# Kernel optimization log

Measured on AMD Instinct MI355X. Metric: run time of the kernel, lower is better.

Reference implementation:

```python
import jax, jax.numpy as jnp
import numpy as np

NUM_HEADS = 16
ROPE_THETA = 10000.0


def _rope_angles(seq_len, head_dim, dtype):
    # lucidrains rotary_embedding_torch: freqs = theta^(-2i/d) for i in 0..d/2,
    # angles = pos * freq, then each angle repeated twice along last dim (interleaved pairs).
    inv_freq = 1.0 / (ROPE_THETA ** (jnp.arange(0, head_dim, 2, dtype=jnp.float32) / head_dim))
    angles = jnp.arange(seq_len, dtype=jnp.float32)[:, None] * inv_freq  # [N, D/2]
    return jnp.repeat(angles, 2, axis=-1).astype(dtype)  # [N, D]


def _rotate_half(t):
    # interleaved pairs: (x0, x1) -> (-x1, x0)
    t1 = t[..., ::2]
    t2 = t[..., 1::2]
    return jnp.stack([-t2, t1], axis=-1).reshape(t.shape)


def _apply_rope(t, cos, sin):
    # t: [B, H, N, D]; cos/sin: [N, D]
    return t * cos + _rotate_half(t) * sin


def setup_inputs() -> dict:
    key = jax.random.key(0)
    ks = jax.random.split(key, 5)
    B, N, C = 4, 1024, 1024
    return {
        "x": jax.random.normal(ks[0], (B, N, C), dtype=jnp.float32),
        "w_qkv": jax.random.normal(ks[1], (C, 3 * C), dtype=jnp.float32) * (C ** -0.5),
        "b_qkv": jax.random.normal(ks[2], (3 * C,), dtype=jnp.float32) * 0.02,
        "w_proj": jax.random.normal(ks[3], (C, C), dtype=jnp.float32) * (C ** -0.5),
        "b_proj": jax.random.normal(ks[4], (C,), dtype=jnp.float32) * 0.02,
    }


def reference(x, w_qkv, b_qkv, w_proj, b_proj):
    B, N, C = x.shape
    H = NUM_HEADS
    D = C // H

    qkv = x @ w_qkv + b_qkv  # [B, N, 3C]
    qkv = qkv.reshape(B, N, 3, H, D).transpose(2, 0, 3, 1, 4)  # [3, B, H, N, D]
    q, k, v = qkv[0], qkv[1], qkv[2]

    ang = _rope_angles(N, D, x.dtype)
    cos, sin = jnp.cos(ang), jnp.sin(ang)
    q = _apply_rope(q, cos, sin)
    k = _apply_rope(k, cos, sin)

    scale = D ** -0.5  # SDPA default scale
    scores = jnp.einsum("bhqd,bhkd->bhqk", q, k) * scale
    attn = jax.nn.softmax(scores, axis=-1)
    out = jnp.einsum("bhqk,bhkd->bhqd", attn, v)  # [B, H, N, D]

    out = out.transpose(0, 2, 1, 3).reshape(B, N, C)
    return out @ w_proj + b_proj
```

## Files before the change

### kernel.cpp

```cpp
#include <hip/hip_runtime.h>
#include <math.h>

#define BB 4
#define NN 1024
#define CC 1024
#define HH 16
#define DD 64
#define N3 3072

typedef __attribute__((ext_vector_type(8))) short bf16x8;
typedef __attribute__((ext_vector_type(8))) _Float16 f16x8;
typedef __attribute__((ext_vector_type(4))) _Float16 f16x4;
typedef __attribute__((ext_vector_type(4))) float f32x4;
typedef __attribute__((ext_vector_type(4))) unsigned int u32x4;
typedef __attribute__((ext_vector_type(2))) unsigned int u32x2;

struct ushort4_t { unsigned short x, y, z, w; };

static __device__ __forceinline__ unsigned short f2b(float f) {
    union { float f; unsigned int u; } v; v.f = f;
    unsigned int r = (v.u + 0x7fffu + ((v.u >> 16) & 1u)) >> 16;
    return (unsigned short)r;
}

static __device__ __forceinline__ void ldg_lds16(const void* g, void* l) {
    __builtin_amdgcn_global_load_lds(
        (const __attribute__((address_space(1))) unsigned int*)g,
        (__attribute__((address_space(3))) unsigned int*)l, 16, 0, 0);
}

static __device__ __forceinline__ void barx()  { asm volatile("s_barrier" ::: "memory"); }
static __device__ __forceinline__ void wlg0()  { asm volatile("s_waitcnt lgkmcnt(0)" ::: "memory");
                                                 __builtin_amdgcn_sched_barrier(0); }
static __device__ __forceinline__ void wvm8()  { asm volatile("s_waitcnt vmcnt(8)" ::: "memory"); }
static __device__ __forceinline__ void wvm4()  { asm volatile("s_waitcnt vmcnt(4)" ::: "memory"); }
static __device__ __forceinline__ void wvm0()  { asm volatile("s_waitcnt vmcnt(0)" ::: "memory"); }
static __device__ __forceinline__ void wnone() {}

__global__ __launch_bounds__(256) void prep(const float* __restrict__ x,
                                            const float* __restrict__ wq,
                                            const float* __restrict__ wp,
                                            _Float16* __restrict__ Xh,
                                            _Float16* __restrict__ Wqt,
                                            _Float16* __restrict__ Wpt,
                                            float* __restrict__ ct,
                                            float* __restrict__ st) {
    __shared__ __align__(16) _Float16 T[64][72];
    const int blk = blockIdx.x;
    const int t = threadIdx.x;
    if (blk < 4096) {
        int tid = blk * 256 + t;
        float4 v = ((const float4*)x)[tid];
        f16x4 o = {(_Float16)v.x, (_Float16)v.y, (_Float16)v.z, (_Float16)v.w};
        ((f16x4*)Xh)[tid] = o;
    } else if (blk < 5120) {
        const float* src; _Float16* dst; int ns, k0, n0;
        if (blk < 4864) {
            int idx = blk - 4096;
            k0 = (idx & 15) * 64; n0 = (idx >> 4) * 64;
            src = wq; dst = Wqt; ns = N3;
        } else {
            int idx = blk - 4864;
            k0 = (idx & 15) * 64; n0 = (idx >> 4) * 64;
            src = wp; dst = Wpt; ns = 1024;
        }
        {
            const int r  = t >> 2;
            const int cf = (t & 3) * 16;
            const float* sp = src + (size_t)(k0 + r) * ns + n0 + cf;
            float4 v0 = *(const float4*)(sp);
            float4 v1 = *(const float4*)(sp + 4);
            float4 v2 = *(const float4*)(sp + 8);
            float4 v3 = *(const float4*)(sp + 12);
            f16x8 a, b;
            a[0]=(_Float16)v0.x; a[1]=(_Float16)v0.y; a[2]=(_Float16)v0.z; a[3]=(_Float16)v0.w;
            a[4]=(_Float16)v1.x; a[5]=(_Float16)v1.y; a[6]=(_Float16)v1.z; a[7]=(_Float16)v1.w;
            b[0]=(_Float16)v2.x; b[1]=(_Float16)v2.y; b[2]=(_Float16)v2.z; b[3]=(_Float16)v2.w;
            b[4]=(_Float16)v3.x; b[5]=(_Float16)v3.y; b[6]=(_Float16)v3.z; b[7]=(_Float16)v3.w;
            *(f16x8*)&T[r][cf]     = a;
            *(f16x8*)&T[r][cf + 8] = b;
        }
        __syncthreads();
        {
            const int n  = t >> 2;
            const int kc = t & 3;
            f16x8 o0, o1;
            #pragma unroll
            for (int kk = 0; kk < 8; kk++) o0[kk] = T[kc * 16 + kk][n];
            #pragma unroll
            for (int kk = 0; kk < 8; kk++) o1[kk] = T[kc * 16 + 8 + kk][n];
            _Float16* dp = dst + (size_t)(n0 + n) * 1024 + k0 + kc * 16;
            *(f16x8*)dp       = o0;
            *(f16x8*)(dp + 8) = o1;
        }
    } else {
        int tid = (blk - 5120) * 256 + t;
        int n = tid >> 5, i = tid & 31;
        double ang = (double)n * exp2(-(double)i * (13.287712379549449 / 32.0));
        ct[tid] = (float)cos(ang);
        st[tid] = (float)sin(ang);
    }
}

__global__ __launch_bounds__(512, 2) void qkv_mfma(const _Float16* __restrict__ Ah,
                                                   const _Float16* __restrict__ Bt,
                                                   const float* __restrict__ bias,
                                                   const float* __restrict__ cost,
                                                   const float* __restrict__ sint,
                                                   unsigned short* __restrict__ Q,
                                                   unsigned short* __restrict__ K,
                                                   unsigned short* __restrict__ Vtg) {
    __shared__ __align__(16) _Float16 LA[4][128 * 64];
    __shared__ __align__(16) _Float16 LB[4][128 * 64];

    const int t    = threadIdx.x;
    const int lane = t & 63;
    const int w    = t >> 6;
    const int ln   = lane & 15, qd = lane >> 4;
    const int n0   = blockIdx.x * 256;
    const int m0   = blockIdx.y * 256;
    const int wm   = (w >> 2) * 128;
    const int wn   = (w & 3) * 64;

    const int L0 = t >> 3, hc0 = (t & 7) ^ (L0 & 7);
    const int row0 = 2 * L0 + (hc0 >> 2), co0 = (hc0 & 3) * 16;
    const int pp = 512 + t;
    const int L1 = pp >> 3, hc1 = (pp & 7) ^ (L1 & 7);
    const int row1 = 2 * L1 + (hc1 >> 2), co1 = (hc1 & 3) * 16;

    const char* gA = (const char*)Ah;
    const char* gB = (const char*)Bt;
    const size_t aof0 = (size_t)(m0 + row0) * 2048 + co0;
    const size_t aof1 = (size_t)(m0 + row1) * 2048 + co1;
    const size_t bof0 = (size_t)(n0 + row0) * 2048 + co0;
    const size_t bof1 = (size_t)(n0 + row1) * 2048 + co1;
    const int ld0 = (w * 64) * 8;
    const int ld1 = (512 + w * 64) * 8;

#define STAGE_A(kk, SLOT) { ldg_lds16(gA + aof0 + (size_t)(kk) * 64, &LA[SLOT][ld0]); \
                            ldg_lds16(gA + aof1 + (size_t)(kk) * 64, &LA[SLOT][ld1]); }
#define STAGE_B(kk, SLOT) { ldg_lds16(gB + bof0 + (size_t)(kk) * 64, &LB[SLOT][ld0]); \
                            ldg_lds16(gB + bof1 + (size_t)(kk) * 64, &LB[SLOT][ld1]); }

    STAGE_A(0, 0); STAGE_B(0, 0);
    STAGE_A(1, 1); STAGE_B(1, 1);
    STAGE_A(2, 2); STAGE_B(2, 2);
    wvm8();
    barx();

    f32x4 acc[8][4];
    #pragma unroll
    for (int i = 0; i < 8; i++)
        #pragma unroll
        for (int j = 0; j < 4; j++) acc[i][j] = (f32x4){0.f, 0.f, 0.f, 0.f};

    auto frag = [&](const _Float16* Lb, int r, int c) -> f16x8 {
        int idx = ((r >> 1) << 6) + ((((((r & 1) << 2) | c)) ^ ((r >> 1) & 7)) << 3);
        return *(const f16x8*)&Lb[idx];
    };

#define QK_TILE(kk, SLOT, STG, WAITFN) {                                            \
    const _Float16* Ab = LA[SLOT];                                                  \
    const _Float16* Bb = LB[SLOT];                                                  \
    f16x8 af[4], bf[4];                                                             \
    _Pragma("unroll") for (int i = 0; i < 4; i++) af[i] = frag(Ab, wm + i * 16 + ln, qd); \
    _Pragma("unroll") for (int j = 0; j < 4; j++) bf[j] = frag(Bb, wn + j * 16 + ln, qd); \
    if (STG) STAGE_A((kk) + 3, ((kk) + 3) & 3);                                     \
    barx(); wlg0();                                                                 \
    __builtin_amdgcn_s_setprio(1);                                                  \
    _Pragma("unroll") for (int i = 0; i < 4; i++)                                   \
        _Pragma("unroll") for (int j = 0; j < 4; j++)                               \
            acc[i][j] = __builtin_amdgcn_mfma_f32_16x16x32_f16(af[i], bf[j], acc[i][j], 0, 0, 0); \
    __builtin_amdgcn_s_setprio(0);                                                  \
    barx();                                                                         \
    _Pragma("unroll") for (int i = 0; i < 4; i++) af[i] = frag(Ab, wm + 64 + i * 16 + ln, qd); \
    if (STG) STAGE_B((kk) + 3, ((kk) + 3) & 3);                                     \
    WAITFN();                                                                       \
    barx(); wlg0();                                                                 \
    __builtin_amdgcn_s_setprio(1);                                                  \
    _Pragma("unroll") for (int i = 0; i < 4; i++)                                   \
        _Pragma("unroll") for (int j = 0; j < 4; j++)                               \
            acc[4 + i][j] = __builtin_amdgcn_mfma_f32_16x16x32_f16(af[i], bf[j], acc[4 + i][j], 0, 0, 0); \
    __builtin_amdgcn_s_setprio(0);                                                  \
    barx();                                                                         \
}

    for (int k = 0; k < 28; k += 4) {
        QK_TILE(k + 0, 0, 1, wvm8);
        QK_TILE(k + 1, 1, 1, wvm8);
        QK_TILE(k + 2, 2, 1, wvm8);
        QK_TILE(k + 3, 3, 1, wvm8);
    }
    QK_TILE(28, 0, 1, wvm8);
    QK_TILE(29, 1, 0, wvm4);
    QK_TILE(30, 2, 0, wvm0);
    QK_TILE(31, 3, 0, wnone);

#undef QK_TILE
#undef STAGE_A
#undef STAGE_B

    float* LW = (float*)(&LA[0][0]) + w * (16 * 68);
    const int s = (n0 + wn) >> 10;
    const int h = ((n0 + wn) >> 6) & 15;
    const int erow = lane >> 2;
    const int ec0  = (lane & 3) * 16;

    if (s < 2) {
        unsigned short* dst = (s == 0) ? Q : K;
        const float sc0 = (s == 0) ? 0.125f : 1.0f;
        f32x4 bb0 = *(const f32x4*)&bias[n0 + wn + ec0 + 0];
        f32x4 bb1 = *(const f32x4*)&bias[n0 + wn + ec0 + 4];
        f32x4 bb2 = *(const f32x4*)&bias[n0 + wn + ec0 + 8];
        f32x4 bb3 = *(const f32x4*)&bias[n0 + wn + ec0 + 12];
        #pragma unroll
        for (int i = 0; i < 8; i++) {
            #pragma unroll
            for (int j = 0; j < 4; j++)
                #pragma unroll
                for (int reg = 0; reg < 4; reg++)
                    LW[(qd * 4 + reg) * 68 + j * 16 + ln] = acc[i][j][reg];
            wlg0();
            f32x4 v0 = *(const f32x4*)&LW[erow * 68 + ec0 + 0];
            f32x4 v1 = *(const f32x4*)&LW[erow * 68 + ec0 + 4];
            f32x4 v2 = *(const f32x4*)&LW[erow * 68 + ec0 + 8];
            f32x4 v3 = *(const f32x4*)&LW[erow * 68 + ec0 + 12];
            wlg0();
            int row = m0 + wm + i * 16 + erow;
            int b = row >> 10, n = row & 1023;
            f32x4 cs0 = *(const f32x4*)&cost[n * 32 + (ec0 >> 1)];
            f32x4 cs1 = *(const f32x4*)&cost[n * 32 + (ec0 >> 1) + 4];
            f32x4 sn0 = *(const f32x4*)&sint[n * 32 + (ec0 >> 1)];
            f32x4 sn1 = *(const f32x4*)&sint[n * 32 + (ec0 >> 1) + 4];
            cs0 *= sc0; cs1 *= sc0; sn0 *= sc0; sn1 *= sc0;
            v0 += bb0; v1 += bb1; v2 += bb2; v3 += bb3;
            unsigned int pk0, pk1, pk2, pk3, pk4, pk5, pk6, pk7;
#define RP(PK, ve, vo, cs, sn) { float oe = (ve) * (cs) - (vo) * (sn);              \
                                 float oo = (vo) * (cs) + (ve) * (sn);              \
            asm("v_cvt_pk_bf16_f32 %0, %1, %2" : "=v"(PK) : "v"(oe), "v"(oo)); }
            RP(pk0, v0[0], v0[1], cs0[0], sn0[0]);
            RP(pk1, v0[2], v0[3], cs0[1], sn0[1]);
            RP(pk2, v1[0], v1[1], cs0[2], sn0[2]);
            RP(pk3, v1[2], v1[3], cs0[3], sn0[3]);
            RP(pk4, v2[0], v2[1], cs1[0], sn1[0]);
            RP(pk5, v2[2], v2[3], cs1[1], sn1[1]);
            RP(pk6, v3[0], v3[1], cs1[2], sn1[2]);
            RP(pk7, v3[2], v3[3], cs1[3], sn1[3]);
#undef RP
            unsigned short* op = dst + (((size_t)(b * HH + h)) * NN + n) * DD + ec0;
            u32x4 o0; o0[0] = pk0; o0[1] = pk1; o0[2] = pk2; o0[3] = pk3;
            u32x4 o1; o1[0] = pk4; o1[1] = pk5; o1[2] = pk6; o1[3] = pk7;
            *(u32x4*)op = o0;
            *(u32x4*)(op + 8) = o1;
        }
    } else {
        const float bb = bias[n0 + wn + lane];
        #pragma unroll
        for (int i = 0; i < 8; i++) {
            #pragma unroll
            for (int j = 0; j < 4; j++)
                #pragma unroll
                for (int reg = 0; reg < 4; reg++)
                    LW[(qd * 4 + reg) * 68 + j * 16 + ln] = acc[i][j][reg];
            wlg0();
            float e0  = LW[ 0 * 68 + lane] + bb, e1  = LW[ 1 * 68 + lane] + bb;
            float e2  = LW[ 2 * 68 + lane] + bb, e3  = LW[ 3 * 68 + lane] + bb;
            float e4  = LW[ 4 * 68 + lane] + bb, e5  = LW[ 5 * 68 + lane] + bb;
            float e6  = LW[ 6 * 68 + lane] + bb, e7  = LW[ 7 * 68 + lane] + bb;
            float e8  = LW[ 8 * 68 + lane] + bb, e9  = LW[ 9 * 68 + lane] + bb;
            float e10 = LW[10 * 68 + lane] + bb, e11 = LW[11 * 68 + lane] + bb;
            float e12 = LW[12 * 68 + lane] + bb, e13 = LW[13 * 68 + lane] + bb;
            float e14 = LW[14 * 68 + lane] + bb, e15 = LW[15 * 68 + lane] + bb;
            wlg0();
            unsigned int pk0, pk1, pk2, pk3, pk4, pk5, pk6, pk7;
#define CV(PK, a, b_) asm("v_cvt_pk_bf16_f32 %0, %1, %2" : "=v"(PK) : "v"(a), "v"(b_))
            CV(pk0, e0,  e1);  CV(pk1, e2,  e3);
            CV(pk2, e4,  e5);  CV(pk3, e6,  e7);
            CV(pk4, e8,  e9);  CV(pk5, e10, e11);
            CV(pk6, e12, e13); CV(pk7, e14, e15);
#undef CV
            int row0v = m0 + wm + i * 16;
            int b = row0v >> 10, nn = row0v & 1023;
            unsigned short* vp = Vtg + ((size_t)(b * HH + h) * DD + lane) * NN + nn;
            u32x4 o0; o0[0] = pk0; o0[1] = pk1; o0[2] = pk2; o0[3] = pk3;
            u32x4 o1; o1[0] = pk4; o1[1] = pk5; o1[2] = pk6; o1[3] = pk7;
            *(u32x4*)vp = o0;
            *(u32x4*)(vp + 8) = o1;
        }
    }
}

static __device__ __forceinline__ void gemm_body_pipe_n64(const char* gA, const char* gB,
                                                          int m0, int n0,
                                                          _Float16* As0, _Float16* As1,
                                                          _Float16* Bs0, _Float16* Bs1,
                                                          int tid, int ln, int qd,
                                                          int wm, int wn, f32x4 acc[4][2]) {
    const int lrow   = tid >> 3;
    const int lchunk = tid & 7;
    const int swz    = (lchunk ^ (lrow & 7)) * 8;

    u32x4 pa[4], pb[2];

    #pragma unroll
    for (int c = 0; c < 4; c++)
        pa[c] = *(const u32x4*)(gA + (size_t)(m0 + c * 32 + lrow) * 2048 + lchunk * 16);
    #pragma unroll
    for (int c = 0; c < 2; c++)
        pb[c] = *(const u32x4*)(gB + (size_t)(n0 + c * 32 + lrow) * 2048 + lchunk * 16);
    #pragma unroll
    for (int c = 0; c < 4; c++)
        *(u32x4*)&As0[(c * 32 + lrow) * 64 + swz] = pa[c];
    #pragma unroll
    for (int c = 0; c < 2; c++)
        *(u32x4*)&Bs0[(c * 32 + lrow) * 64 + swz] = pb[c];
    #pragma unroll
    for (int c = 0; c < 4; c++)
        pa[c] = *(const u32x4*)(gA + (size_t)(m0 + c * 32 + lrow) * 2048 + 128 + lchunk * 16);
    #pragma unroll
    for (int c = 0; c < 2; c++)
        pb[c] = *(const u32x4*)(gB + (size_t)(n0 + c * 32 + lrow) * 2048 + 128 + lchunk * 16);
    __syncthreads();

    #pragma unroll
    for (int t = 0; t < 16; t++) {
        const _Float16* Ac = (t & 1) ? As1 : As0;
        const _Float16* Bc = (t & 1) ? Bs1 : Bs0;

        #pragma unroll
        for (int kc = 0; kc < 2; kc++) {
            f16x8 af[4], bf[2];
            #pragma unroll
            for (int i = 0; i < 4; i++)
                af[i] = *(const f16x8*)&Ac[(wm + i * 16 + ln) * 64 +
                                           (((kc * 4 + qd) ^ (ln & 7)) * 8)];
            #pragma unroll
            for (int j = 0; j < 2; j++)
                bf[j] = *(const f16x8*)&Bc[(wn + j * 16 + ln) * 64 +
                                           (((kc * 4 + qd) ^ (ln & 7)) * 8)];
            #pragma unroll
            for (int i = 0; i < 4; i++)
                #pragma unroll
                for (int j = 0; j < 2; j++)
                    acc[i][j] = __builtin_amdgcn_mfma_f32_16x16x32_f16(af[i], bf[j],
                                                                       acc[i][j], 0, 0, 0);
        }

        if (t < 15) {
            _Float16* An = (t & 1) ? As0 : As1;
            _Float16* Bn = (t & 1) ? Bs0 : Bs1;
            #pragma unroll
            for (int c = 0; c < 4; c++)
                *(u32x4*)&An[(c * 32 + lrow) * 64 + swz] = pa[c];
            #pragma unroll
            for (int c = 0; c < 2; c++)
                *(u32x4*)&Bn[(c * 32 + lrow) * 64 + swz] = pb[c];
            if (t < 14) {
                size_t ko = (size_t)(t + 2) * 128;
                #pragma unroll
                for (int c = 0; c < 4; c++)
                    pa[c] = *(const u32x4*)(gA + (size_t)(m0 + c * 32 + lrow) * 2048 + ko + lchunk * 16);
                #pragma unroll
                for (int c = 0; c < 2; c++)
                    pb[c] = *(const u32x4*)(gB + (size_t)(n0 + c * 32 + lrow) * 2048 + ko + lchunk * 16);
            }
        }
        __syncthreads();
    }
}

__global__ __launch_bounds__(256, 3) void attn_flash(const unsigned short* __restrict__ Qb,
                                                     const unsigned short* __restrict__ Kb,
                                                     const unsigned short* __restrict__ Vtg,
                                                     _Float16* __restrict__ AO) {
    __shared__ __align__(16) unsigned short Ks[2][64 * 64];
    __shared__ __align__(16) unsigned short Vt[2][64 * 64];
    __shared__ __align__(16) unsigned short Ps[4][32 * 64];

    const int t    = threadIdx.x;
    const int lane = t & 63;
    const int w    = t >> 6;
    const int ln   = lane & 15;
    const int qd   = lane >> 4;

    const int lin  = blockIdx.x;
    const int slot = lin >> 3;
    const int hb   = (lin & 7) + 8 * (slot & 7);
    const int bq   = slot >> 3;
    const int h    = hb & 15;
    const int b    = hb >> 4;

    const size_t base = (size_t)(b * HH + h) * NN * DD;
    const char* Kc = (const char*)(Kb + base);
    const char* Vc = (const char*)(Vtg + base);
    const int xorc = ((lane & 7) ^ (lane >> 3)) * 16;
    const int r8   = lane >> 3;
    const int wrow = w * 16;

    bf16x8 qf[2][2];
    #pragma unroll
    for (int g = 0; g < 2; g++) {
        const unsigned short* qp = Qb + base +
            (size_t)(bq * 128 + w * 32 + g * 16 + ln) * DD + qd * 8;
        qf[g][0] = *(const bf16x8*)qp;
        qf[g][1] = *(const bf16x8*)(qp + 32);
    }

    f32x4 o[2][5];
    #pragma unroll
    for (int g = 0; g < 2; g++)
        #pragma unroll
        for (int x = 0; x < 5; x++) o[g][x] = (f32x4){0.f, 0.f, 0.f, 0.f};

    bf16x8 onesf;
    #pragma unroll
    for (int x = 0; x < 8; x++) onesf[x] = (short)0x3F80;

#define STAGE_K(tile, buf) {                                                     \
    _Pragma("unroll") for (int c = 0; c < 2; c++) {                              \
        int rr = wrow + c * 8 + r8;                                              \
        ldg_lds16(Kc + (size_t)((tile) * 64 + rr) * 128 + xorc,                  \
                  &Ks[buf][(wrow + c * 8) * 64]);                                \
    } }
// ... 57 lines not shown
        }

        {
            bf16x8 pf[2][2];
            #pragma unroll
            for (int g = 0; g < 2; g++) {
                pf[g][0] = *(const bf16x8*)&PsB[(g * 16 + ln) * 64 + ((qd ^ (ln & 7)) * 8)];
                pf[g][1] = *(const bf16x8*)&PsB[(g * 16 + ln) * 64 + (((4 + qd) ^ (ln & 7)) * 8)];
            }
            __builtin_amdgcn_s_setprio(1);
            #pragma unroll
            for (int j = 0; j < 4; j++) {
                bf16x8 v0f = *(const bf16x8*)&VtB[(ln + 16 * j) * 64 + ((qd ^ (ln & 7)) * 8)];
                bf16x8 v1f = *(const bf16x8*)&VtB[(ln + 16 * j) * 64 + (((4 + qd) ^ (ln & 7)) * 8)];
                #pragma unroll
                for (int g = 0; g < 2; g++) {
                    o[g][j] = __builtin_amdgcn_mfma_f32_16x16x32_bf16(pf[g][0], v0f, o[g][j], 0, 0, 0);
                    o[g][j] = __builtin_amdgcn_mfma_f32_16x16x32_bf16(pf[g][1], v1f, o[g][j], 0, 0, 0);
                }
            }
            #pragma unroll
            for (int g = 0; g < 2; g++) {
                o[g][4] = __builtin_amdgcn_mfma_f32_16x16x32_bf16(pf[g][0], onesf, o[g][4], 0, 0, 0);
                o[g][4] = __builtin_amdgcn_mfma_f32_16x16x32_bf16(pf[g][1], onesf, o[g][4], 0, 0, 0);
            }
            __builtin_amdgcn_s_setprio(0);
        }

        barx();

        if (tt < 14) {
            STAGE_K(tt + 2, tt & 1);
            STAGE_V(tt + 2, tt & 1);
        }
    }

#undef STAGE_K
#undef STAGE_V

    #pragma unroll
    for (int g = 0; g < 2; g++)
        #pragma unroll
        for (int r = 0; r < 4; r++) {
            float inv = __builtin_amdgcn_rcpf(o[g][4][r]);
            int q = bq * 128 + w * 32 + g * 16 + qd * 4 + r;
            _Float16* op = AO + (((size_t)b * NN + q) * HH + h) * DD + ln;
            op[0]  = (_Float16)(o[g][0][r] * inv);
            op[16] = (_Float16)(o[g][1][r] * inv);
            op[32] = (_Float16)(o[g][2][r] * inv);
            op[48] = (_Float16)(o[g][3][r] * inv);
        }
}

__global__ __launch_bounds__(256) void proj_mfma(const _Float16* __restrict__ Ah,
                                                 const _Float16* __restrict__ Bt,
                                                 const float* __restrict__ bias,
                                                 float* __restrict__ out) {
    __shared__ __align__(16) _Float16 As[2][128 * 64];
    __shared__ __align__(16) _Float16 Bs[2][64 * 64];
    const int t = threadIdx.x;
    const int lane = t & 63;
    const int w = t >> 6;
    const int ln = lane & 15, qd = lane >> 4;
    const int n0 = blockIdx.x * 64;
    const int m0 = blockIdx.y * 128;
    const int wm = (w >> 1) * 64, wn = (w & 1) * 32;

    f32x4 acc[4][2];
    #pragma unroll
    for (int i = 0; i < 4; i++)
        #pragma unroll
        for (int j = 0; j < 2; j++) acc[i][j] = (f32x4){0.f, 0.f, 0.f, 0.f};

    gemm_body_pipe_n64((const char*)Ah, (const char*)Bt, m0, n0,
                       As[0], As[1], Bs[0], Bs[1], t, ln, qd, wm, wn, acc);

    #pragma unroll
    for (int i = 0; i < 4; i++) {
        #pragma unroll
        for (int reg = 0; reg < 4; reg++) {
            int row = m0 + wm + i * 16 + qd * 4 + reg;
            #pragma unroll
            for (int j = 0; j < 2; j++) {
                int col = n0 + wn + j * 16 + ln;
                out[(size_t)row * 1024 + col] = acc[i][j][reg] + bias[col];
            }
        }
    }
}

extern "C" void kernel_launch(void* const* d_in, const int* in_sizes, int n_in,
                              void* d_out, int out_size, void* d_ws, size_t ws_size,
                              hipStream_t stream) {
    const float* x      = (const float*)d_in[0];
    const float* w_qkv  = (const float*)d_in[1];
    const float* b_qkv  = (const float*)d_in[2];
    const float* w_proj = (const float*)d_in[3];
    const float* b_proj = (const float*)d_in[4];
    float* out = (float*)d_out;

    char* ws = (char*)d_ws;
    _Float16* Xh   = (_Float16*)(ws);
    _Float16* Wqt  = (_Float16*)(ws + (8u << 20));
    _Float16* Wpt  = (_Float16*)(ws + (14u << 20));
    unsigned short* Q  = (unsigned short*)(ws + (16u << 20));
    unsigned short* K  = (unsigned short*)(ws + (24u << 20));
    unsigned short* Vt = (unsigned short*)(ws + (32u << 20));
    _Float16* AOh  = (_Float16*)(ws + (40u << 20));
    float* cost    = (float*)(ws + (48u << 20));
    float* sint    = (float*)(ws + (48u << 20) + (128u << 10));

    prep<<<5248, 256, 0, stream>>>(x, w_qkv, w_proj, Xh, Wqt, Wpt, cost, sint);
    qkv_mfma<<<dim3(12, 16), 512, 0, stream>>>(Xh, Wqt, b_qkv, cost, sint, Q, K, Vt);
    attn_flash<<<512, 256, 0, stream>>>(Q, K, Vt, AOh);
    proj_mfma<<<dim3(16, 32), 256, 0, stream>>>(AOh, Wpt, b_proj, out);
}
```

Before: 164.7 us.

## Retile QKV GEMM to 128x384 blocks with direct-register epilogue

Changes the QKV projection GEMM tile from 256x256 to 128x384 per block, raising the grid from 192 to 256 blocks so more CUs are busy, and merges the two half-tile MFMA phases into one per k-step. The epilogue no longer stages accumulators through LDS. It applies bias and RoPE per element, using a lane shuffle for the rotation pair, and writes scalar bf16 stores for Q/K and 4-element stores for transposed V. In exchange, the epilogue issues many narrow, poorly coalesced global stores and per-element cos/sin loads, and each block reloads its A tile more often.

```diff
diff --git a/kernel.cpp b/kernel.cpp
--- a/kernel.cpp
+++ b/kernel.cpp
@@ -110,49 +110,51 @@
                                                    unsigned short* __restrict__ Q,
                                                    unsigned short* __restrict__ K,
                                                    unsigned short* __restrict__ Vtg) {
-    __shared__ __align__(16) _Float16 LA[4][128 * 64];
-    __shared__ __align__(16) _Float16 LB[4][128 * 64];
+    __shared__ __align__(16) _Float16 LA[4][128 * 32];
+    __shared__ __align__(16) _Float16 LB[4][384 * 32];
 
     const int t    = threadIdx.x;
     const int lane = t & 63;
     const int w    = t >> 6;
     const int ln   = lane & 15, qd = lane >> 4;
-    const int n0   = blockIdx.x * 256;
-    const int m0   = blockIdx.y * 256;
-    const int wm   = (w >> 2) * 128;
-    const int wn   = (w & 3) * 64;
-
-    const int L0 = t >> 3, hc0 = (t & 7) ^ (L0 & 7);
-    const int row0 = 2 * L0 + (hc0 >> 2), co0 = (hc0 & 3) * 16;
-    const int pp = 512 + t;
-    const int L1 = pp >> 3, hc1 = (pp & 7) ^ (L1 & 7);
-    const int row1 = 2 * L1 + (hc1 >> 2), co1 = (hc1 & 3) * 16;
+    const int n0   = blockIdx.x * 384;
+    const int m0   = blockIdx.y * 128;
+    const int wm   = (w >> 2) * 64;
+    const int wn   = (w & 3) * 96;
+
+    const int La = t >> 3, ha = (t & 7) ^ (La & 7);
+    const int rowA = 2 * La + (ha >> 2), coA = (ha & 3) * 16;
+    const int p1 = 512 + t,  Lb1 = p1 >> 3, hb1 = (p1 & 7) ^ (Lb1 & 7);
+    const int p2 = 1024 + t, Lb2 = p2 >> 3, hb2 = (p2 & 7) ^ (Lb2 & 7);
+    const int rowB0 = 2 * La  + (ha  >> 2), coB0 = (ha  & 3) * 16;
+    const int rowB1 = 2 * Lb1 + (hb1 >> 2), coB1 = (hb1 & 3) * 16;
+    const int rowB2 = 2 * Lb2 + (hb2 >> 2), coB2 = (hb2 & 3) * 16;
 
     const char* gA = (const char*)Ah;
     const char* gB = (const char*)Bt;
-    const size_t aof0 = (size_t)(m0 + row0) * 2048 + co0;
-    const size_t aof1 = (size_t)(m0 + row1) * 2048 + co1;
-    const size_t bof0 = (size_t)(n0 + row0) * 2048 + co0;
-    const size_t bof1 = (size_t)(n0 + row1) * 2048 + co1;
-    const int ld0 = (w * 64) * 8;
-    const int ld1 = (512 + w * 64) * 8;
-
-#define STAGE_A(kk, SLOT) { ldg_lds16(gA + aof0 + (size_t)(kk) * 64, &LA[SLOT][ld0]); \
-                            ldg_lds16(gA + aof1 + (size_t)(kk) * 64, &LA[SLOT][ld1]); }
-#define STAGE_B(kk, SLOT) { ldg_lds16(gB + bof0 + (size_t)(kk) * 64, &LB[SLOT][ld0]); \
-                            ldg_lds16(gB + bof1 + (size_t)(kk) * 64, &LB[SLOT][ld1]); }
-
-    STAGE_A(0, 0); STAGE_B(0, 0);
-    STAGE_A(1, 1); STAGE_B(1, 1);
-    STAGE_A(2, 2); STAGE_B(2, 2);
+    const size_t aof  = (size_t)(m0 + rowA)  * 2048 + coA;
+    const size_t bof0 = (size_t)(n0 + rowB0) * 2048 + coB0;
+    const size_t bof1 = (size_t)(n0 + rowB1) * 2048 + coB1;
+    const size_t bof2 = (size_t)(n0 + rowB2) * 2048 + coB2;
+    const int ldA  = (w * 64) * 8;
+    const int ldB0 = (w * 64) * 8;
+    const int ldB1 = (512 + w * 64) * 8;
+    const int ldB2 = (1024 + w * 64) * 8;
+
+#define STAGE(kk, SLOT) { ldg_lds16(gA + aof  + (size_t)(kk) * 64, &LA[SLOT][ldA]);  \
+                          ldg_lds16(gB + bof0 + (size_t)(kk) * 64, &LB[SLOT][ldB0]); \
+                          ldg_lds16(gB + bof1 + (size_t)(kk) * 64, &LB[SLOT][ldB1]); \
+                          ldg_lds16(gB + bof2 + (size_t)(kk) * 64, &LB[SLOT][ldB2]); }
+
+    STAGE(0, 0); STAGE(1, 1); STAGE(2, 2);
     wvm8();
     barx();
 
-    f32x4 acc[8][4];
-    #pragma unroll
-    for (int i = 0; i < 8; i++)
-        #pragma unroll
-        for (int j = 0; j < 4; j++) acc[i][j] = (f32x4){0.f, 0.f, 0.f, 0.f};
+    f32x4 acc[4][6];
+    #pragma unroll
+    for (int i = 0; i < 4; i++)
+        #pragma unroll
+        for (int j = 0; j < 6; j++) acc[i][j] = (f32x4){0.f, 0.f, 0.f, 0.f};
 
     auto frag = [&](const _Float16* Lb, int r, int c) -> f16x8 {
         int idx = ((r >> 1) << 6) + ((((((r & 1) << 2) | c)) ^ ((r >> 1) & 7)) << 3);
@@ -162,25 +164,16 @@
 #define QK_TILE(kk, SLOT, STG, WAITFN) {                                            \
     const _Float16* Ab = LA[SLOT];                                                  \
     const _Float16* Bb = LB[SLOT];                                                  \
-    f16x8 af[4], bf[4];                                                             \
+    f16x8 af[4], bf[6];                                                             \
     _Pragma("unroll") for (int i = 0; i < 4; i++) af[i] = frag(Ab, wm + i * 16 + ln, qd); \
-    _Pragma("unroll") for (int j = 0; j < 4; j++) bf[j] = frag(Bb, wn + j * 16 + ln, qd); \
-    if (STG) STAGE_A((kk) + 3, ((kk) + 3) & 3);                                     \
+    _Pragma("unroll") for (int j = 0; j < 6; j++) bf[j] = frag(Bb, wn + j * 16 + ln, qd); \
+    if (STG) STAGE((kk) + 3, ((kk) + 3) & 3);                                       \
+    WAITFN();               \
     barx(); wlg0();                                                                 \
     __builtin_amdgcn_s_setprio(1);                                                  \
     _Pragma("unroll") for (int i = 0; i < 4; i++)                                   \
-        _Pragma("unroll") for (int j = 0; j < 4; j++)                               \
+        _Pragma("unroll") for (int j = 0; j < 6; j++)                               \
             acc[i][j] = __builtin_amdgcn_mfma_f32_16x16x32_f16(af[i], bf[j], acc[i][j], 0, 0, 0); \
-    __builtin_amdgcn_s_setprio(0);                                                  \
-    barx();                                                                         \
-    _Pragma("unroll") for (int i = 0; i < 4; i++) af[i] = frag(Ab, wm + 64 + i * 16 + ln, qd); \
-    if (STG) STAGE_B((kk) + 3, ((kk) + 3) & 3);                                     \
-    WAITFN();                                                                       \
-    barx(); wlg0();                                                                 \
-    __builtin_amdgcn_s_setprio(1);                                                  \
-    _Pragma("unroll") for (int i = 0; i < 4; i++)                                   \
-        _Pragma("unroll") for (int j = 0; j < 4; j++)                               \
-            acc[4 + i][j] = __builtin_amdgcn_mfma_f32_16x16x32_f16(af[i], bf[j], acc[4 + i][j], 0, 0, 0); \
     __builtin_amdgcn_s_setprio(0);                                                  \
     barx();                                                                         \
 }
@@ -197,95 +190,47 @@
     QK_TILE(31, 3, 0, wnone);
 
 #undef QK_TILE
-#undef STAGE_A
-#undef STAGE_B
-
-    float* LW = (float*)(&LA[0][0]) + w * (16 * 68);
-    const int s = (n0 + wn) >> 10;
-    const int h = ((n0 + wn) >> 6) & 15;
-    const int erow = lane >> 2;
-    const int ec0  = (lane & 3) * 16;
-
-    if (s < 2) {
-        unsigned short* dst = (s == 0) ? Q : K;
-        const float sc0 = (s == 0) ? 0.125f : 1.0f;
-        f32x4 bb0 = *(const f32x4*)&bias[n0 + wn + ec0 + 0];
-        f32x4 bb1 = *(const f32x4*)&bias[n0 + wn + ec0 + 4];
-        f32x4 bb2 = *(const f32x4*)&bias[n0 + wn + ec0 + 8];
-        f32x4 bb3 = *(const f32x4*)&bias[n0 + wn + ec0 + 12];
-        #pragma unroll
-        for (int i = 0; i < 8; i++) {
-            #pragma unroll
-            for (int j = 0; j < 4; j++)
+#undef STAGE
+
+    #pragma unroll
+    for (int j = 0; j < 6; j++) {
+        const int coln = n0 + wn + j * 16;
+        const int s  = coln >> 10;
+        const int h  = (coln >> 6) & 15;
+        const int d0 = coln & 63;
+        const float bb = bias[coln + ln];
+        if (s < 2) {
+            unsigned short* dst = (s == 0) ? Q : K;
+            const float sc0 = (s == 0) ? 0.125f : 1.0f;
+            const int d = d0 + ln;
+            #pragma unroll
+            for (int i = 0; i < 4; i++) {
                 #pragma unroll
-                for (int reg = 0; reg < 4; reg++)
-                    LW[(qd * 4 + reg) * 68 + j * 16 + ln] = acc[i][j][reg];
-            wlg0();
-            f32x4 v0 = *(const f32x4*)&LW[erow * 68 + ec0 + 0];
-            f32x4 v1 = *(const f32x4*)&LW[erow * 68 + ec0 + 4];
-            f32x4 v2 = *(const f32x4*)&LW[erow * 68 + ec0 + 8];
-            f32x4 v3 = *(const f32x4*)&LW[erow * 68 + ec0 + 12];
-            wlg0();
-            int row = m0 + wm + i * 16 + erow;
-            int b = row >> 10, n = row & 1023;
-            f32x4 cs0 = *(const f32x4*)&cost[n * 32 + (ec0 >> 1)];
-            f32x4 cs1 = *(const f32x4*)&cost[n * 32 + (ec0 >> 1) + 4];
-            f32x4 sn0 = *(const f32x4*)&sint[n * 32 + (ec0 >> 1)];
-            f32x4 sn1 = *(const f32x4*)&sint[n * 32 + (ec0 >> 1) + 4];
-            cs0 *= sc0; cs1 *= sc0; sn0 *= sc0; sn1 *= sc0;
-            v0 += bb0; v1 += bb1; v2 += bb2; v3 += bb3;
-            unsigned int pk0, pk1, pk2, pk3, pk4, pk5, pk6, pk7;
-#define RP(PK, ve, vo, cs, sn) { float oe = (ve) * (cs) - (vo) * (sn);              \
-                                 float oo = (vo) * (cs) + (ve) * (sn);              \
-            asm("v_cvt_pk_bf16_f32 %0, %1, %2" : "=v"(PK) : "v"(oe), "v"(oo)); }
-            RP(pk0, v0[0], v0[1], cs0[0], sn0[0]);
-            RP(pk1, v0[2], v0[3], cs0[1], sn0[1]);
-            RP(pk2, v1[0], v1[1], cs0[2], sn0[2]);
-            RP(pk3, v1[2], v1[3], cs0[3], sn0[3]);
-            RP(pk4, v2[0], v2[1], cs1[0], sn1[0]);
-            RP(pk5, v2[2], v2[3], cs1[1], sn1[1]);
-            RP(pk6, v3[0], v3[1], cs1[2], sn1[2]);
-            RP(pk7, v3[2], v3[3], cs1[3], sn1[3]);
-#undef RP
-            unsigned short* op = dst + (((size_t)(b * HH + h)) * NN + n) * DD + ec0;
-            u32x4 o0; o0[0] = pk0; o0[1] = pk1; o0[2] = pk2; o0[3] = pk3;
-            u32x4 o1; o1[0] = pk4; o1[1] = pk5; o1[2] = pk6; o1[3] = pk7;
-            *(u32x4*)op = o0;
-            *(u32x4*)(op + 8) = o1;
-        }
-    } else {
-        const float bb = bias[n0 + wn + lane];
-        #pragma unroll
-        for (int i = 0; i < 8; i++) {
-            #pragma unroll
-            for (int j = 0; j < 4; j++)
-                #pragma unroll
-                for (int reg = 0; reg < 4; reg++)
-                    LW[(qd * 4 + reg) * 68 + j * 16 + ln] = acc[i][j][reg];
-            wlg0();
-            float e0  = LW[ 0 * 68 + lane] + bb, e1  = LW[ 1 * 68 + lane] + bb;
-            float e2  = LW[ 2 * 68 + lane] + bb, e3  = LW[ 3 * 68 + lane] + bb;
-            float e4  = LW[ 4 * 68 + lane] + bb, e5  = LW[ 5 * 68 + lane] + bb;
-            float e6  = LW[ 6 * 68 + lane] + bb, e7  = LW[ 7 * 68 + lane] + bb;
-            float e8  = LW[ 8 * 68 + lane] + bb, e9  = LW[ 9 * 68 + lane] + bb;
-            float e10 = LW[10 * 68 + lane] + bb, e11 = LW[11 * 68 + lane] + bb;
-            float e12 = LW[12 * 68 + lane] + bb, e13 = LW[13 * 68 + lane] + bb;
-            float e14 = LW[14 * 68 + lane] + bb, e15 = LW[15 * 68 + lane] + bb;
-            wlg0();
-            unsigned int pk0, pk1, pk2, pk3, pk4, pk5, pk6, pk7;
-#define CV(PK, a, b_) asm("v_cvt_pk_bf16_f32 %0, %1, %2" : "=v"(PK) : "v"(a), "v"(b_))
-            CV(pk0, e0,  e1);  CV(pk1, e2,  e3);
-            CV(pk2, e4,  e5);  CV(pk3, e6,  e7);
-            CV(pk4, e8,  e9);  CV(pk5, e10, e11);
-            CV(pk6, e12, e13); CV(pk7, e14, e15);
-#undef CV
-            int row0v = m0 + wm + i * 16;
-            int b = row0v >> 10, nn = row0v & 1023;
-            unsigned short* vp = Vtg + ((size_t)(b * HH + h) * DD + lane) * NN + nn;
-            u32x4 o0; o0[0] = pk0; o0[1] = pk1; o0[2] = pk2; o0[3] = pk3;
-            u32x4 o1; o1[0] = pk4; o1[1] = pk5; o1[2] = pk6; o1[3] = pk7;
-            *(u32x4*)vp = o0;
-            *(u32x4*)(vp + 8) = o1;
+                for (int reg = 0; reg < 4; reg++) {
+                    int row = m0 + wm + i * 16 + qd * 4 + reg;
+                    int b = row >> 10, n = row & 1023;
+                    float v = acc[i][j][reg] + bb;
+                    float pv = __shfl_xor(v, 1);
+                    float cs = cost[n * 32 + (d >> 1)];
+                    float sn = sint[n * 32 + (d >> 1)];
+                    float outv = ((d & 1) ? (v * cs + pv * sn) : (v * cs - pv * sn)) * sc0;
+                    dst[(((size_t)(b * HH + h)) * NN + n) * DD + d] = f2b(outv);
+                }
+            }
+        } else {
+            const int d = d0 + ln;
+            #pragma unroll
+            for (int i = 0; i < 4; i++) {
+                int row0 = m0 + wm + i * 16 + qd * 4;
+                int b = row0 >> 10, n = row0 & 1023;
+                size_t tbase = ((size_t)(b * HH + h)) * DD * NN + n;
+                ushort4_t pk;
+                pk.x = f2b(acc[i][j][0] + bb);
+                pk.y = f2b(acc[i][j][1] + bb);
+                pk.z = f2b(acc[i][j][2] + bb);
+                pk.w = f2b(acc[i][j][3] + bb);
+                *(ushort4_t*)&Vtg[tbase + (size_t)d * NN] = pk;
+            }
         }
     }
 }
@@ -591,7 +536,7 @@
     float* sint    = (float*)(ws + (48u << 20) + (128u << 10));
 
     prep<<<5248, 256, 0, stream>>>(x, w_qkv, w_proj, Xh, Wqt, Wpt, cost, sint);
-    qkv_mfma<<<dim3(12, 16), 512, 0, stream>>>(Xh, Wqt, b_qkv, cost, sint, Q, K, Vt);
+    qkv_mfma<<<dim3(8, 32), 512, 0, stream>>>(Xh, Wqt, b_qkv, cost, sint, Q, K, Vt);
     attn_flash<<<512, 256, 0, stream>>>(Q, K, Vt, AOh);
     proj_mfma<<<dim3(16, 32), 256, 0, stream>>>(AOh, Wpt, b_proj, out);
 }
```

After: 168.9 us. 1.03x slower.

## Restructure QKV GEMM main loop to double-buffered K=64 tiles with half-tile staging

Applied to the files above, without the earlier changes.

The QKV projection GEMM now uses a 2-stage double buffer of K=64 tiles, each split into two 128-row halves, instead of a 4-deep ring of K=32 tiles. Loads for the next tile are issued per half, interleaved with the MFMA phases, and each wave reads fragments for a 128x64 sub-tile in four quadrant steps with a new swizzle. The aim is fewer barriers and iterations per K and better overlap of global-to-LDS loads with MFMA. The trade-off is shallower prefetch depth (one tile ahead), which may expose memory latency.

```diff
diff --git a/kernel.cpp b/kernel.cpp
--- a/kernel.cpp
+++ b/kernel.cpp
@@ -32,10 +32,8 @@
 static __device__ __forceinline__ void barx()  { asm volatile("s_barrier" ::: "memory"); }
 static __device__ __forceinline__ void wlg0()  { asm volatile("s_waitcnt lgkmcnt(0)" ::: "memory");
                                                  __builtin_amdgcn_sched_barrier(0); }
-static __device__ __forceinline__ void wvm8()  { asm volatile("s_waitcnt vmcnt(8)" ::: "memory"); }
 static __device__ __forceinline__ void wvm4()  { asm volatile("s_waitcnt vmcnt(4)" ::: "memory"); }
 static __device__ __forceinline__ void wvm0()  { asm volatile("s_waitcnt vmcnt(0)" ::: "memory"); }
-static __device__ __forceinline__ void wnone() {}
 
 __global__ __launch_bounds__(256) void prep(const float* __restrict__ x,
                                             const float* __restrict__ wq,
@@ -110,8 +108,8 @@
                                                    unsigned short* __restrict__ Q,
                                                    unsigned short* __restrict__ K,
                                                    unsigned short* __restrict__ Vtg) {
-    __shared__ __align__(16) _Float16 LA[4][128 * 64];
-    __shared__ __align__(16) _Float16 LB[4][128 * 64];
+    __shared__ __align__(16) _Float16 LA[2][2][128 * 64];
+    __shared__ __align__(16) _Float16 LB[2][2][128 * 64];
 
     const int t    = threadIdx.x;
     const int lane = t & 63;
@@ -121,32 +119,29 @@
     const int m0   = blockIdx.y * 256;
     const int wm   = (w >> 2) * 128;
     const int wn   = (w & 3) * 64;
-
-    const int L0 = t >> 3, hc0 = (t & 7) ^ (L0 & 7);
-    const int row0 = 2 * L0 + (hc0 >> 2), co0 = (hc0 & 3) * 16;
-    const int pp = 512 + t;
-    const int L1 = pp >> 3, hc1 = (pp & 7) ^ (L1 & 7);
-    const int row1 = 2 * L1 + (hc1 >> 2), co1 = (hc1 & 3) * 16;
-
+    const int ah   = w >> 2;
+    const int bh   = (w & 3) >> 1;
+    const int wnl  = (w & 1) * 64;
+
+    const int srow = t >> 3;
+    const int scg  = (t & 7) ^ (srow & 7);
     const char* gA = (const char*)Ah;
     const char* gB = (const char*)Bt;
-    const size_t aof0 = (size_t)(m0 + row0) * 2048 + co0;
-    const size_t aof1 = (size_t)(m0 + row1) * 2048 + co1;
-    const size_t bof0 = (size_t)(n0 + row0) * 2048 + co0;
-    const size_t bof1 = (size_t)(n0 + row1) * 2048 + co1;
-    const int ld0 = (w * 64) * 8;
-    const int ld1 = (512 + w * 64) * 8;
-
-#define STAGE_A(kk, SLOT) { ldg_lds16(gA + aof0 + (size_t)(kk) * 64, &LA[SLOT][ld0]); \
-                            ldg_lds16(gA + aof1 + (size_t)(kk) * 64, &LA[SLOT][ld1]); }
-#define STAGE_B(kk, SLOT) { ldg_lds16(gB + bof0 + (size_t)(kk) * 64, &LB[SLOT][ld0]); \
-                            ldg_lds16(gB + bof1 + (size_t)(kk) * 64, &LB[SLOT][ld1]); }
-
-    STAGE_A(0, 0); STAGE_B(0, 0);
-    STAGE_A(1, 1); STAGE_B(1, 1);
-    STAGE_A(2, 2); STAGE_B(2, 2);
-    wvm8();
-    barx();
+    const size_t aSrc = (size_t)(m0 + srow) * 2048 + scg * 16;
+    const size_t bSrc = (size_t)(n0 + srow) * 2048 + scg * 16;
+    const int ldsOff = w * 1024;
+
+#define STAGE_AH(kk, hh, dd) {                                                      \
+    char* lb = (char*)&LA[dd][hh][0] + ldsOff;                                      \
+    ldg_lds16(gA + aSrc + (size_t)(hh) * 262144 + (size_t)(kk) * 128, lb);          \
+    ldg_lds16(gA + aSrc + (size_t)(hh) * 262144 + 131072 + (size_t)(kk) * 128, lb + 8192); }
+#define STAGE_BH(kk, hh, dd) {                                                      \
+    char* lb = (char*)&LB[dd][hh][0] + ldsOff;                                      \
+    ldg_lds16(gB + bSrc + (size_t)(hh) * 262144 + (size_t)(kk) * 128, lb);          \
+    ldg_lds16(gB + bSrc + (size_t)(hh) * 262144 + 131072 + (size_t)(kk) * 128, lb + 8192); }
+
+    STAGE_AH(0, 0, 0); STAGE_AH(0, 1, 0);
+    STAGE_BH(0, 0, 0); STAGE_BH(0, 1, 0);
 
     f32x4 acc[8][4];
     #pragma unroll
@@ -154,53 +149,70 @@
         #pragma unroll
         for (int j = 0; j < 4; j++) acc[i][j] = (f32x4){0.f, 0.f, 0.f, 0.f};
 
-    auto frag = [&](const _Float16* Lb, int r, int c) -> f16x8 {
-        int idx = ((r >> 1) << 6) + ((((((r & 1) << 2) | c)) ^ ((r >> 1) & 7)) << 3);
-        return *(const f16x8*)&Lb[idx];
-    };
-
-#define QK_TILE(kk, SLOT, STG, WAITFN) {                                            \
-    const _Float16* Ab = LA[SLOT];                                                  \
-    const _Float16* Bb = LB[SLOT];                                                  \
-    f16x8 af[4], bf[4];                                                             \
-    _Pragma("unroll") for (int i = 0; i < 4; i++) af[i] = frag(Ab, wm + i * 16 + ln, qd); \
-    _Pragma("unroll") for (int j = 0; j < 4; j++) bf[j] = frag(Bb, wn + j * 16 + ln, qd); \
-    if (STG) STAGE_A((kk) + 3, ((kk) + 3) & 3);                                     \
+    f16x8 af[4][2], bf0[2][2], bf1[2][2];
+
+    const int sc0  = ((qd) ^ (ln & 7)) * 16;
+    const int sc1  = ((4 + qd) ^ (ln & 7)) * 16;
+    const int aRow = ln * 128;
+    const int bRow = (wnl + ln) * 128;
+
+#define RD_AF(AB, MI) {                                                             \
+    const char* ab_ = (AB) + (MI) * 8192 + aRow;                                    \
+    _Pragma("unroll") for (int i = 0; i < 4; i++) {                                 \
+        af[i][0] = *(const f16x8*)(ab_ + i * 2048 + sc0);                           \
+        af[i][1] = *(const f16x8*)(ab_ + i * 2048 + sc1); } }
+#define RD_BF(BBp, NJ, DST) {                                                       \
+    const char* bb_ = (BBp) + (NJ) * 4096 + bRow;                                   \
+    _Pragma("unroll") for (int j = 0; j < 2; j++) {                                 \
+        DST[j][0] = *(const f16x8*)(bb_ + j * 2048 + sc0);                          \
+        DST[j][1] = *(const f16x8*)(bb_ + j * 2048 + sc1); } }
+#define MM(MI, NJ, BFS)                                                             \
+    _Pragma("unroll") for (int kc = 0; kc < 2; kc++)                                \
+    _Pragma("unroll") for (int i = 0; i < 4; i++)                                   \
+    _Pragma("unroll") for (int j = 0; j < 2; j++)                                   \
+        acc[(MI) * 4 + i][(NJ) * 2 + j] = __builtin_amdgcn_mfma_f32_16x16x32_f16(   \
+            af[i][kc], BFS[j][kc], acc[(MI) * 4 + i][(NJ) * 2 + j], 0, 0, 0);
+
+#define QTILE(kk, dd, LAST) {                                                       \
+    const char* Ahb = (const char*)&LA[dd][ah][0];                                  \
+    const char* Bhb = (const char*)&LB[dd][bh][0];                                  \
+                   \
+    if (!(LAST)) { STAGE_AH((kk) + 1, 0, (dd) ^ 1); STAGE_BH((kk) + 1, 0, (dd) ^ 1); } \
+    if (!(LAST)) wvm4(); else wvm0();                                               \
+    barx();                                                                         \
+    RD_AF(Ahb, 0); RD_BF(Bhb, 0, bf0);                                              \
+    wlg0();                                                                         \
+    __builtin_amdgcn_s_setprio(1); MM(0, 0, bf0); __builtin_amdgcn_s_setprio(0);    \
+    barx();                                                                         \
+                             \
+    RD_BF(Bhb, 1, bf1);                                                             \
+    if (!(LAST)) { STAGE_AH((kk) + 1, 1, (dd) ^ 1); STAGE_BH((kk) + 1, 1, (dd) ^ 1); } \
     barx(); wlg0();                                                                 \
-    __builtin_amdgcn_s_setprio(1);                                                  \
-    _Pragma("unroll") for (int i = 0; i < 4; i++)                                   \
-        _Pragma("unroll") for (int j = 0; j < 4; j++)                               \
-            acc[i][j] = __builtin_amdgcn_mfma_f32_16x16x32_f16(af[i], bf[j], acc[i][j], 0, 0, 0); \
+    __builtin_amdgcn_s_setprio(1); MM(0, 1, bf1); __builtin_amdgcn_s_setprio(0);    \
+    barx();                                                                         \
+                                     \
+    RD_AF(Ahb, 1);                                                                  \
+    barx(); wlg0();                                                                 \
+    __builtin_amdgcn_s_setprio(1); MM(1, 1, bf1); MM(1, 0, bf0);                    \
     __builtin_amdgcn_s_setprio(0);                                                  \
     barx();                                                                         \
-    _Pragma("unroll") for (int i = 0; i < 4; i++) af[i] = frag(Ab, wm + 64 + i * 16 + ln, qd); \
-    if (STG) STAGE_B((kk) + 3, ((kk) + 3) & 3);                                     \
-    WAITFN();                                                                       \
-    barx(); wlg0();                                                                 \
-    __builtin_amdgcn_s_setprio(1);                                                  \
-    _Pragma("unroll") for (int i = 0; i < 4; i++)                                   \
-        _Pragma("unroll") for (int j = 0; j < 4; j++)                               \
-            acc[4 + i][j] = __builtin_amdgcn_mfma_f32_16x16x32_f16(af[i], bf[j], acc[4 + i][j], 0, 0, 0); \
-    __builtin_amdgcn_s_setprio(0);                                                  \
-    barx();                                                                         \
-}
-
-    for (int k = 0; k < 28; k += 4) {
-        QK_TILE(k + 0, 0, 1, wvm8);
-        QK_TILE(k + 1, 1, 1, wvm8);
-        QK_TILE(k + 2, 2, 1, wvm8);
-        QK_TILE(k + 3, 3, 1, wvm8);
+}
+
+    for (int kk = 0; kk < 14; kk += 2) {
+        QTILE(kk,     0, 0);
+        QTILE(kk + 1, 1, 0);
     }
-    QK_TILE(28, 0, 1, wvm8);
-    QK_TILE(29, 1, 0, wvm4);
-    QK_TILE(30, 2, 0, wvm0);
-    QK_TILE(31, 3, 0, wnone);
-
-#undef QK_TILE
-#undef STAGE_A
-#undef STAGE_B
-
-    float* LW = (float*)(&LA[0][0]) + w * (16 * 68);
+    QTILE(14, 0, 0);
+    QTILE(15, 1, 1);
+
+#undef QTILE
+#undef MM
+#undef RD_AF
+#undef RD_BF
+#undef STAGE_AH
+#undef STAGE_BH
+
+    float* LW = (float*)(&LA[0][0][0]) + w * (16 * 68);
     const int s = (n0 + wn) >> 10;
     const int h = ((n0 + wn) >> 6) & 15;
     const int erow = lane >> 2;
@@ -208,7 +220,7 @@
 
     if (s < 2) {
         unsigned short* dst = (s == 0) ? Q : K;
-        const float sc0 = (s == 0) ? 0.125f : 1.0f;
+        const float sc0f = (s == 0) ? 0.125f : 1.0f;
         f32x4 bb0 = *(const f32x4*)&bias[n0 + wn + ec0 + 0];
         f32x4 bb1 = *(const f32x4*)&bias[n0 + wn + ec0 + 4];
         f32x4 bb2 = *(const f32x4*)&bias[n0 + wn + ec0 + 8];
@@ -232,7 +244,7 @@
             f32x4 cs1 = *(const f32x4*)&cost[n * 32 + (ec0 >> 1) + 4];
             f32x4 sn0 = *(const f32x4*)&sint[n * 32 + (ec0 >> 1)];
             f32x4 sn1 = *(const f32x4*)&sint[n * 32 + (ec0 >> 1) + 4];
-            cs0 *= sc0; cs1 *= sc0; sn0 *= sc0; sn1 *= sc0;
+            cs0 *= sc0f; cs1 *= sc0f; sn0 *= sc0f; sn1 *= sc0f;
             v0 += bb0; v1 += bb1; v2 += bb2; v3 += bb3;
             unsigned int pk0, pk1, pk2, pk3, pk4, pk5, pk6, pk7;
 #define RP(PK, ve, vo, cs, sn) { float oe = (ve) * (cs) - (vo) * (sn);              \
@@ -280,8 +292,8 @@
             CV(pk6, e12, e13); CV(pk7, e14, e15);
 #undef CV
             int row0v = m0 + wm + i * 16;
-            int b = row0v >> 10, nn = row0v & 1023;
-            unsigned short* vp = Vtg + ((size_t)(b * HH + h) * DD + lane) * NN + nn;
+            int b = row0v >> 10, nn2 = row0v & 1023;
+            unsigned short* vp = Vtg + ((size_t)(b * HH + h) * DD + lane) * NN + nn2;
             u32x4 o0; o0[0] = pk0; o0[1] = pk1; o0[2] = pk2; o0[3] = pk3;
             u32x4 o1; o1[0] = pk4; o1[1] = pk5; o1[2] = pk6; o1[3] = pk7;
             *(u32x4*)vp = o0;
```

Result: slower. 169.4 us (+2.9%).

## Rewrite output projection GEMM with async global-to-LDS 4-stage pipeline and larger tiles

Applied to the files above, without the earlier changes.

The projection GEMM now uses 512-thread blocks computing 128x128 tiles, down from 256 threads on 128x64. Global data is loaded straight into LDS through global_load_lds in a 4-slot ring with K-step 32, and waits are paced with explicit vmcnt counts and barriers. Wave priority is raised around the MFMA block, and bias loads are hoisted out of the store loop. The intent is to cut register round-trips and load latency stalls and to reuse more data per tile. The cost is fewer blocks (256) and two barriers per k-step.

```diff
diff --git a/kernel.cpp b/kernel.cpp
--- a/kernel.cpp
+++ b/kernel.cpp
@@ -34,6 +34,7 @@
                                                  __builtin_amdgcn_sched_barrier(0); }
 static __device__ __forceinline__ void wvm8()  { asm volatile("s_waitcnt vmcnt(8)" ::: "memory"); }
 static __device__ __forceinline__ void wvm4()  { asm volatile("s_waitcnt vmcnt(4)" ::: "memory"); }
+static __device__ __forceinline__ void wvm2()  { asm volatile("s_waitcnt vmcnt(2)" ::: "memory"); }
 static __device__ __forceinline__ void wvm0()  { asm volatile("s_waitcnt vmcnt(0)" ::: "memory"); }
 static __device__ __forceinline__ void wnone() {}
 
@@ -290,85 +291,6 @@
     }
 }
 
-static __device__ __forceinline__ void gemm_body_pipe_n64(const char* gA, const char* gB,
-                                                          int m0, int n0,
-                                                          _Float16* As0, _Float16* As1,
-                                                          _Float16* Bs0, _Float16* Bs1,
-                                                          int tid, int ln, int qd,
-                                                          int wm, int wn, f32x4 acc[4][2]) {
-    const int lrow   = tid >> 3;
-    const int lchunk = tid & 7;
-    const int swz    = (lchunk ^ (lrow & 7)) * 8;
-
-    u32x4 pa[4], pb[2];
-
-    #pragma unroll
-    for (int c = 0; c < 4; c++)
-        pa[c] = *(const u32x4*)(gA + (size_t)(m0 + c * 32 + lrow) * 2048 + lchunk * 16);
-    #pragma unroll
-    for (int c = 0; c < 2; c++)
-        pb[c] = *(const u32x4*)(gB + (size_t)(n0 + c * 32 + lrow) * 2048 + lchunk * 16);
-    #pragma unroll
-    for (int c = 0; c < 4; c++)
-        *(u32x4*)&As0[(c * 32 + lrow) * 64 + swz] = pa[c];
-    #pragma unroll
-    for (int c = 0; c < 2; c++)
-        *(u32x4*)&Bs0[(c * 32 + lrow) * 64 + swz] = pb[c];
-    #pragma unroll
-    for (int c = 0; c < 4; c++)
-        pa[c] = *(const u32x4*)(gA + (size_t)(m0 + c * 32 + lrow) * 2048 + 128 + lchunk * 16);
-    #pragma unroll
-    for (int c = 0; c < 2; c++)
-        pb[c] = *(const u32x4*)(gB + (size_t)(n0 + c * 32 + lrow) * 2048 + 128 + lchunk * 16);
-    __syncthreads();
-
-    #pragma unroll
-    for (int t = 0; t < 16; t++) {
-        const _Float16* Ac = (t & 1) ? As1 : As0;
-        const _Float16* Bc = (t & 1) ? Bs1 : Bs0;
-
-        #pragma unroll
-        for (int kc = 0; kc < 2; kc++) {
-            f16x8 af[4], bf[2];
-            #pragma unroll
-            for (int i = 0; i < 4; i++)
-                af[i] = *(const f16x8*)&Ac[(wm + i * 16 + ln) * 64 +
-                                           (((kc * 4 + qd) ^ (ln & 7)) * 8)];
-            #pragma unroll
-            for (int j = 0; j < 2; j++)
-                bf[j] = *(const f16x8*)&Bc[(wn + j * 16 + ln) * 64 +
-                                           (((kc * 4 + qd) ^ (ln & 7)) * 8)];
-            #pragma unroll
-            for (int i = 0; i < 4; i++)
-                #pragma unroll
-                for (int j = 0; j < 2; j++)
-                    acc[i][j] = __builtin_amdgcn_mfma_f32_16x16x32_f16(af[i], bf[j],
-                                                                       acc[i][j], 0, 0, 0);
-        }
-
-        if (t < 15) {
-            _Float16* An = (t & 1) ? As0 : As1;
-            _Float16* Bn = (t & 1) ? Bs0 : Bs1;
-            #pragma unroll
-            for (int c = 0; c < 4; c++)
-                *(u32x4*)&An[(c * 32 + lrow) * 64 + swz] = pa[c];
-            #pragma unroll
-            for (int c = 0; c < 2; c++)
-                *(u32x4*)&Bn[(c * 32 + lrow) * 64 + swz] = pb[c];
-            if (t < 14) {
-                size_t ko = (size_t)(t + 2) * 128;
-                #pragma unroll
-                for (int c = 0; c < 4; c++)
-                    pa[c] = *(const u32x4*)(gA + (size_t)(m0 + c * 32 + lrow) * 2048 + ko + lchunk * 16);
-                #pragma unroll
-                for (int c = 0; c < 2; c++)
-                    pb[c] = *(const u32x4*)(gB + (size_t)(n0 + c * 32 + lrow) * 2048 + ko + lchunk * 16);
-            }
-        }
-        __syncthreads();
-    }
-}
-
 __global__ __launch_bounds__(256, 3) void attn_flash(const unsigned short* __restrict__ Qb,
                                                      const unsigned short* __restrict__ Kb,
                                                      const unsigned short* __restrict__ Vtg,
@@ -532,19 +454,36 @@
         }
 }
 
-__global__ __launch_bounds__(256) void proj_mfma(const _Float16* __restrict__ Ah,
-                                                 const _Float16* __restrict__ Bt,
-                                                 const float* __restrict__ bias,
-                                                 float* __restrict__ out) {
-    __shared__ __align__(16) _Float16 As[2][128 * 64];
-    __shared__ __align__(16) _Float16 Bs[2][64 * 64];
-    const int t = threadIdx.x;
+__global__ __launch_bounds__(512, 2) void proj_mfma(const _Float16* __restrict__ Ah,
+                                                    const _Float16* __restrict__ Bt,
+                                                    const float* __restrict__ bias,
+                                                    float* __restrict__ out) {
+    __shared__ __align__(16) _Float16 LA[4][128 * 32];
+    __shared__ __align__(16) _Float16 LB[4][128 * 32];
+
+    const int t    = threadIdx.x;
     const int lane = t & 63;
-    const int w = t >> 6;
-    const int ln = lane & 15, qd = lane >> 4;
-    const int n0 = blockIdx.x * 64;
-    const int m0 = blockIdx.y * 128;
-    const int wm = (w >> 1) * 64, wn = (w & 1) * 32;
+    const int w    = t >> 6;
+    const int ln   = lane & 15, qd = lane >> 4;
+    const int n0   = blockIdx.x * 128;
+    const int m0   = blockIdx.y * 128;
+    const int wm   = (w >> 2) * 64;
+    const int wn   = (w & 3) * 32;
+
+    const int L  = t >> 3, hc = (t & 7) ^ (L & 7);
+    const int row = 2 * L + (hc >> 2), co = (hc & 3) * 16;
+    const char* gA = (const char*)Ah;
+    const char* gB = (const char*)Bt;
+    const size_t aof = (size_t)(m0 + row) * 2048 + co;
+    const size_t bof = (size_t)(n0 + row) * 2048 + co;
+    const int ld = (w * 64) * 8;
+
+#define PSTAGE(kk, SLOT) { ldg_lds16(gA + aof + (size_t)(kk) * 64, &LA[SLOT][ld]); \
+                           ldg_lds16(gB + bof + (size_t)(kk) * 64, &LB[SLOT][ld]); }
+
+    PSTAGE(0, 0); PSTAGE(1, 1); PSTAGE(2, 2);
+    wvm4();
+    barx();
 
     f32x4 acc[4][2];
     #pragma unroll
@@ -552,19 +491,52 @@
         #pragma unroll
         for (int j = 0; j < 2; j++) acc[i][j] = (f32x4){0.f, 0.f, 0.f, 0.f};
 
-    gemm_body_pipe_n64((const char*)Ah, (const char*)Bt, m0, n0,
-                       As[0], As[1], Bs[0], Bs[1], t, ln, qd, wm, wn, acc);
-
+    auto frag = [&](const _Float16* Lb, int r, int c) -> f16x8 {
+        int idx = ((r >> 1) << 6) + ((((((r & 1) << 2) | c)) ^ ((r >> 1) & 7)) << 3);
+        return *(const f16x8*)&Lb[idx];
+    };
+
+#define PTILE(kk, SLOT, STG, WAITFN) {                                              \
+    const _Float16* Ab = LA[SLOT];                                                  \
+    const _Float16* Bb = LB[SLOT];                                                  \
+    f16x8 af[4], bf[2];                                                             \
+    _Pragma("unroll") for (int i = 0; i < 4; i++) af[i] = frag(Ab, wm + i * 16 + ln, qd); \
+    _Pragma("unroll") for (int j = 0; j < 2; j++) bf[j] = frag(Bb, wn + j * 16 + ln, qd); \
+    if (STG) PSTAGE((kk) + 3, ((kk) + 3) & 3);                                      \
+    WAITFN();                                                                       \
+    barx(); wlg0();                                                                 \
+    __builtin_amdgcn_s_setprio(1);                                                  \
+    _Pragma("unroll") for (int i = 0; i < 4; i++)                                   \
+        _Pragma("unroll") for (int j = 0; j < 2; j++)                               \
+            acc[i][j] = __builtin_amdgcn_mfma_f32_16x16x32_f16(af[i], bf[j], acc[i][j], 0, 0, 0); \
+    __builtin_amdgcn_s_setprio(0);                                                  \
+    barx();                                                                         \
+}
+
+    for (int k = 0; k < 28; k += 4) {
+        PTILE(k + 0, 0, 1, wvm4);
+        PTILE(k + 1, 1, 1, wvm4);
+        PTILE(k + 2, 2, 1, wvm4);
+        PTILE(k + 3, 3, 1, wvm4);
+    }
+    PTILE(28, 0, 1, wvm4);
+    PTILE(29, 1, 0, wvm2);
+    PTILE(30, 2, 0, wvm0);
+    PTILE(31, 3, 0, wnone);
+
+#undef PTILE
+#undef PSTAGE
+
+    const float bc0 = bias[n0 + wn + ln];
+    const float bc1 = bias[n0 + wn + 16 + ln];
     #pragma unroll
     for (int i = 0; i < 4; i++) {
         #pragma unroll
         for (int reg = 0; reg < 4; reg++) {
-            int row = m0 + wm + i * 16 + qd * 4 + reg;
-            #pragma unroll
-            for (int j = 0; j < 2; j++) {
-                int col = n0 + wn + j * 16 + ln;
-                out[(size_t)row * 1024 + col] = acc[i][j][reg] + bias[col];
-            }
+            int rowo = m0 + wm + i * 16 + qd * 4 + reg;
+            float* op = out + (size_t)rowo * 1024 + n0 + wn + ln;
+            op[0]  = acc[i][0][reg] + bc0;
+            op[16] = acc[i][1][reg] + bc1;
         }
     }
 }
@@ -593,5 +565,5 @@
     prep<<<5248, 256, 0, stream>>>(x, w_qkv, w_proj, Xh, Wqt, Wpt, cost, sint);
     qkv_mfma<<<dim3(12, 16), 512, 0, stream>>>(Xh, Wqt, b_qkv, cost, sint, Q, K, Vt);
     attn_flash<<<512, 256, 0, stream>>>(Q, K, Vt, AOh);
-    proj_mfma<<<dim3(16, 32), 256, 0, stream>>>(AOh, Wpt, b_proj, out);
-}
+    proj_mfma<<<dim3(8, 32), 512, 0, stream>>>(AOh, Wpt, b_proj, out);
+}
```

After: 161.4 us. -2.0%, faster.
